# Kernel tuning notes

Measured on AMD Instinct MI355X. Metric: run time of the kernel, lower is better.

The kernel has to match this reference:

```python
import jax, jax.numpy as jnp
import numpy as np

N = 100000
IN_DIM = 128
OUT_DIM = 128
E = 320000


def setup_inputs() -> dict:
    key = jax.random.key(0)
    ks = jax.random.split(key, 12)
    x = jax.random.normal(ks[0], (N, IN_DIM), dtype=jnp.float32)
    src0 = jax.random.randint(ks[1], (E,), 0, N)
    dst0 = jax.random.randint(ks[2], (E,), 0, N)
    src1 = jax.random.randint(ks[3], (E,), 0, N)
    dst1 = jax.random.randint(ks[4], (E,), 0, N)
    s = 1.0 / np.sqrt(IN_DIM)
    W0 = jax.random.uniform(ks[5], (IN_DIM, OUT_DIM), minval=-s, maxval=s)
    b0 = jax.random.uniform(ks[6], (OUT_DIM,), minval=-s, maxval=s)
    W1 = jax.random.uniform(ks[7], (IN_DIM, OUT_DIM), minval=-s, maxval=s)
    b1 = jax.random.uniform(ks[8], (OUT_DIM,), minval=-s, maxval=s)
    sa = 1.0 / np.sqrt(2 * OUT_DIM)
    a0 = jax.random.uniform(ks[9], (2 * OUT_DIM,), minval=-sa, maxval=sa)
    a1 = jax.random.uniform(ks[10], (2 * OUT_DIM,), minval=-sa, maxval=sa)
    return {"x": x, "src0": src0, "dst0": dst0, "src1": src1, "dst1": dst1,
            "W0": W0, "b0": b0, "a0": a0, "W1": W1, "b1": b1, "a1": a1}


def _rel_gat(x, src, dst, W, b, a):
    # wh = Linear(in_dim, out_dim)(x)  -> [N, D]
    wh = x @ W + b
    D = wh.shape[1]
    # e = leaky_relu(a^T [wh_src || wh_dst]) ; split a instead of concat on edges
    e = jax.nn.leaky_relu(wh[src] @ a[:D] + wh[dst] @ a[D:])  # [E]
    # segment softmax over incoming edges of each dst node
    m = jax.ops.segment_max(e, dst, num_segments=N)
    ex = jnp.exp(e - m[dst])
    denom = jax.ops.segment_sum(ex, dst, num_segments=N)
    alpha = ex / denom[dst]  # [E]
    # weighted scatter-sum of src features (zero for isolated dst nodes)
    return jax.ops.segment_sum(alpha[:, None] * wh[src], dst, num_segments=N)


def reference(x, src0, dst0, src1, dst1, W0, b0, a0, W1, b1, a1):
    h0 = _rel_gat(x, src0, dst0, W0, b0, a0)
    h1 = _rel_gat(x, src1, dst1, W1, b1, a1)
    # cross-relation 'sum' reducer
    return h0 + h1
```

## Files before the change

### kernel.cpp

```cpp
#include <hip/hip_runtime.h>
#include <hip/hip_bf16.h>


typedef __bf16 bf16x8 __attribute__((ext_vector_type(8)));
typedef float f32x4 __attribute__((ext_vector_type(4)));

#define DIM 128

__global__ __launch_bounds__(256) void prep_w_kernel(
    const float* __restrict__ W0, const float* __restrict__ W1,
    __bf16* __restrict__ wtf)
{
    const int e = blockIdx.x * 256 + threadIdx.x;
    if (e >= 4096) return;
    const int lane = e & 63;
    const int ko4  = (e >> 6) & 3;
    const int ct   = (e >> 8) & 7;
    const int rel  = e >> 11;
    const float* W = rel ? W1 : W0;
    const int n  = ct * 16 + (lane & 15);
    const int k0 = ko4 * 32 + (lane >> 4) * 8;
    bf16x8 v;
#pragma unroll
    for (int j = 0; j < 8; ++j) v[j] = (__bf16)W[(k0 + j) * DIM + n];
    *(bf16x8*)(wtf + (size_t)e * 8) = v;
}

__global__ __launch_bounds__(256) void gemm_wh_kernel(
    const float* __restrict__ x, const __bf16* __restrict__ wtf,
    const float* __restrict__ b0, const float* __restrict__ b1,
    const float* __restrict__ a0, const float* __restrict__ a1,
    const int* __restrict__ dst0, const int* __restrict__ dst1,
    unsigned* __restrict__ deg, unsigned* __restrict__ rank,
    __bf16* __restrict__ wh, float* __restrict__ s_src,
    float* __restrict__ s_dst, int N, int E)
{
    __shared__ __align__(16) __bf16 Cst[64 * 136];
    const int tid = threadIdx.x;

    {
        const int gid = blockIdx.x * 256 + tid;
        if (gid < E) {
            rank[gid]     = atomicAdd(deg + dst0[gid], 1u);
            rank[E + gid] = atomicAdd(deg + N + dst1[gid], 1u);
        }
    }

    const int lane = tid & 63;
    const int wave = tid >> 6;
    const int quad = lane >> 4;
    const int mr   = lane & 15;

    const long row0 = (long)blockIdx.x * 64 + wave * 16;
    long arow = row0 + mr;
    if (arow >= N) arow = N - 1;
    const f32x4* xr = (const f32x4*)(x + arow * DIM);

    bf16x8 afrag[4];
#pragma unroll
    for (int ko4 = 0; ko4 < 4; ++ko4) {
        f32x4 lo = xr[ko4 * 8 + quad * 2], hi = xr[ko4 * 8 + quad * 2 + 1];
        afrag[ko4] = (bf16x8){ (__bf16)lo.x, (__bf16)lo.y, (__bf16)lo.z, (__bf16)lo.w,
                               (__bf16)hi.x, (__bf16)hi.y, (__bf16)hi.z, (__bf16)hi.w };
    }

    const bf16x8* wt = (const bf16x8*)wtf;

#pragma unroll
    for (int rel = 0; rel < 2; ++rel) {
        f32x4 zero = {0.f, 0.f, 0.f, 0.f};
        f32x4 acc[8];
#pragma unroll
        for (int t = 0; t < 8; ++t) acc[t] = zero;

#pragma unroll
        for (int ko4 = 0; ko4 < 4; ++ko4) {
#pragma unroll
            for (int ct = 0; ct < 8; ++ct) {
                bf16x8 bfrag = wt[((rel * 8 + ct) * 4 + ko4) * 64 + lane];
                acc[ct] = __builtin_amdgcn_mfma_f32_16x16x32_bf16(afrag[ko4], bfrag, acc[ct], 0, 0, 0);
            }
        }

        const float* bias = rel ? b1 : b0;
        const float* a    = rel ? a1 : a0;
        float psr[4] = {0.f, 0.f, 0.f, 0.f};
        float pdr[4] = {0.f, 0.f, 0.f, 0.f};
#pragma unroll
        for (int ct = 0; ct < 8; ++ct) {
            const int c = ct * 16 + mr;
            const float bn = bias[c];
            const float asc = a[c], adc = a[DIM + c];
#pragma unroll
            for (int rr = 0; rr < 4; ++rr) {
                const float wv = acc[ct][rr] + bn;
                Cst[(wave * 16 + quad * 4 + rr) * 136 + c] = (__bf16)wv;
                psr[rr] += asc * wv;
                pdr[rr] += adc * wv;
            }
        }
#pragma unroll
        for (int off = 1; off < 16; off <<= 1) {
#pragma unroll
            for (int rr = 0; rr < 4; ++rr) {
                psr[rr] += __shfl_xor(psr[rr], off);
                pdr[rr] += __shfl_xor(pdr[rr], off);
            }
        }
        if (mr == 0) {
#pragma unroll
            for (int rr = 0; rr < 4; ++rr) {
                const long orow = row0 + quad * 4 + rr;
                if (orow < N) {
                    s_src[(size_t)rel * N + orow] = psr[rr];
                    s_dst[(size_t)rel * N + orow] = pdr[rr];
                }
            }
        }
        __syncthreads();
#pragma unroll
        for (int i = 0; i < 4; ++i) {
            const int chunk = tid + 256 * i;
            const int row = chunk >> 4, c8 = chunk & 15;
            bf16x8 v = *(const bf16x8*)&Cst[row * 136 + c8 * 8];
            const long grow = (long)blockIdx.x * 64 + row;
            if (grow < N)
                *(bf16x8*)(wh + ((size_t)rel * N + grow) * DIM + c8 * 8) = v;
        }
        __syncthreads();
    }
}

__global__ __launch_bounds__(256) void scanA_kernel(
    const unsigned* __restrict__ deg, unsigned* __restrict__ tmp,
    unsigned* __restrict__ bsum, int n)
{
    __shared__ unsigned s[256];
    const int t = threadIdx.x;
    const int i = blockIdx.x * 256 + t;
    unsigned v = (i < n) ? deg[i] : 0u;
    s[t] = v;
    __syncthreads();
#pragma unroll
    for (int off = 1; off < 256; off <<= 1) {
        unsigned add = (t >= off) ? s[t - off] : 0u;
        __syncthreads();
        s[t] += add;
        __syncthreads();
    }
    if (i < n) tmp[i] = s[t] - v;
    if (t == 255) bsum[blockIdx.x] = s[t];
}

__global__ __launch_bounds__(256) void scan2_kernel(
    const unsigned* __restrict__ tmp, const unsigned* __restrict__ bsum,
    const unsigned* __restrict__ deg, unsigned* __restrict__ rowptr,
    int n, int nb)
{
    __shared__ unsigned s[256];
    __shared__ unsigned ex[1024];
    const int t = threadIdx.x;
    unsigned loc[4], sum = 0u;
#pragma unroll
    for (int k = 0; k < 4; ++k) {
        int idx = t * 4 + k;
        loc[k] = (idx < nb) ? bsum[idx] : 0u;
        sum += loc[k];
    }
    s[t] = sum;
    __syncthreads();
#pragma unroll
    for (int off = 1; off < 256; off <<= 1) {
        unsigned add = (t >= off) ? s[t - off] : 0u;
        __syncthreads();
        s[t] += add;
        __syncthreads();
    }
    unsigned run = s[t] - sum;
#pragma unroll
    for (int k = 0; k < 4; ++k) {
        ex[t * 4 + k] = run;
        run += loc[k];
    }
    __syncthreads();
    const unsigned pref = ex[blockIdx.x];
    const int i = blockIdx.x * 256 + t;
    if (i < n) {
        unsigned val = tmp[i] + pref;
        rowptr[i] = val;
        if (i == n - 1) rowptr[n] = val + deg[i];
    }
}

__global__ __launch_bounds__(256) void fill_kernel(
    const int* __restrict__ src0, const int* __restrict__ dst0,
    const int* __restrict__ src1, const int* __restrict__ dst1,
    const float* __restrict__ s_src, const float* __restrict__ s_dst,
    const unsigned* __restrict__ rowptr, const unsigned* __restrict__ rank,
    float* __restrict__ denom, uint2* __restrict__ sorted, int N, int E)
{
    const int i = blockIdx.x * 256 + threadIdx.x;
    if (i >= E) return;
    const int s0 = src0[i], d0 = dst0[i];
    const int s1 = src1[i], d1 = dst1[i];
    const unsigned r0 = rank[i], r1 = rank[E + i];
    const unsigned p0 = rowptr[d0] + r0;
    const unsigned p1 = rowptr[N + d1] + r1;

    float v0 = s_src[s0] + s_dst[d0];
    v0 = v0 > 0.f ? v0 : 0.01f * v0;
    const float e0 = __expf(v0);
    float v1 = s_src[N + s1] + s_dst[N + d1];
    v1 = v1 > 0.f ? v1 : 0.01f * v1;
    const float e1 = __expf(v1);

    sorted[p0] = make_uint2((unsigned)s0, __float_as_uint(e0));
    sorted[p1] = make_uint2((unsigned)s1, __float_as_uint(e1));
    atomicAdd(denom + d0, e0);
    atomicAdd(denom + N + d1, e1);
}

__global__ __launch_bounds__(256) void aggregate_kernel(
    const unsigned* __restrict__ rowptr, const uint2* __restrict__ sorted,
    const float* __restrict__ denom, const __bf16* __restrict__ wh,
    float* __restrict__ out, int N)
{
    const int tid  = threadIdx.x;
    const int lane = tid & 63;
    const int sub  = lane >> 4;
    const int mr   = lane & 15;
    int d = blockIdx.x * 4 + (tid >> 6);
    if (d >= N) return;
    d = __builtin_amdgcn_readfirstlane(d);

    const unsigned beg0 = rowptr[d],     end0 = rowptr[d + 1];
    const unsigned beg1 = rowptr[N + d], end1 = rowptr[N + d + 1];
    const unsigned len0 = end0 - beg0;
    const unsigned T    = len0 + (end1 - beg1);
    const float inv0 = (end0 > beg0) ? 1.f / denom[d]     : 0.f;
    const float inv1 = (end1 > beg1) ? 1.f / denom[N + d] : 0.f;

    float o[8];
#pragma unroll
    for (int k = 0; k < 8; ++k) o[k] = 0.f;

    const size_t whstride = (size_t)N * DIM;

    for (unsigned t0 = 0; t0 < T; t0 += 8) {
        const unsigned tA = t0 + sub, tB = tA + 4;
        const bool vA = tA < T, vB = tB < T;
        const bool rA = tA >= len0, rB = tB >= len0;

        unsigned iA = rA ? beg1 + (tA - len0) : beg0 + tA;
        unsigned iB = rB ? beg1 + (tB - len0) : beg0 + tB;
        iA = vA ? iA : 0u;
        iB = vB ? iB : 0u;

        const uint2 eA = sorted[iA];
        const uint2 eB = sorted[iB];

        const float wgtA = vA ? __uint_as_float(eA.y) * (rA ? inv1 : inv0) : 0.f;
        const float wgtB = vB ? __uint_as_float(eB.y) * (rB ? inv1 : inv0) : 0.f;

        const bf16x8 wA = *(const bf16x8*)(wh + (rA ? whstride : 0)
                                              + (size_t)eA.x * DIM + mr * 8);
        const bf16x8 wB = *(const bf16x8*)(wh + (rB ? whstride : 0)
                                              + (size_t)eB.x * DIM + mr * 8);
#pragma unroll
        for (int k = 0; k < 8; ++k) o[k] += wgtA * (float)wA[k];
#pragma unroll
        for (int k = 0; k < 8; ++k) o[k] += wgtB * (float)wB[k];
    }

#pragma unroll
    for (int k = 0; k < 8; ++k) {
        o[k] += __shfl_xor(o[k], 16);
        o[k] += __shfl_xor(o[k], 32);
    }

    if (sub == 0) {
        float4 v0 = {o[0], o[1], o[2], o[3]};
        float4 v1 = {o[4], o[5], o[6], o[7]};
        float* op = out + (size_t)d * DIM + mr * 8;
        *(float4*)op       = v0;
        *(float4*)(op + 4) = v1;
    }
}

extern "C" void kernel_launch(void* const* d_in, const int* in_sizes, int n_in,
                              void* d_out, int out_size, void* d_ws, size_t ws_size,
                              hipStream_t stream) {
    const float* x = (const float*)d_in[0];
    const int* srcs[2] = {(const int*)d_in[1], (const int*)d_in[3]};
    const int* dsts[2] = {(const int*)d_in[2], (const int*)d_in[4]};
    const float* Ws[2] = {(const float*)d_in[5], (const float*)d_in[8]};
    const float* Bs[2] = {(const float*)d_in[6], (const float*)d_in[9]};
    const float* As[2] = {(const float*)d_in[7], (const float*)d_in[10]};

    const int N = in_sizes[0] / DIM;
    const int E = in_sizes[1];
    const int n2 = 2 * N;
    const int nb = (n2 + 255) / 256;
    float* out = (float*)d_out;

    char* p = (char*)d_ws;
    __bf16*   wh     = (__bf16*)p;   p += (size_t)n2 * DIM * 2;
    __bf16*   wtf    = (__bf16*)p;   p += (size_t)4096 * 8 * 2;
    float*    s_src  = (float*)p;    p += (size_t)n2 * 4;
    float*    s_dst  = (float*)p;    p += (size_t)n2 * 4;
    unsigned* deg    = (unsigned*)p; p += (size_t)n2 * 4;
    float*    denom  = (float*)p;    p += (size_t)n2 * 4;
    unsigned* tmp    = (unsigned*)p; p += (size_t)n2 * 4;
    unsigned* rowptr = (unsigned*)p; p += (size_t)(n2 + 2) * 4;
    unsigned* rank   = (unsigned*)p; p += (size_t)2 * E * 4;
    uint2*    sorted = (uint2*)p;    p += (size_t)2 * E * 8;
    unsigned* bsum   = (unsigned*)p; p += (size_t)nb * 4;

    hipMemsetAsync(deg, 0, (size_t)n2 * 4 * 2, stream);
    prep_w_kernel<<<16, 256, 0, stream>>>(Ws[0], Ws[1], wtf);

    gemm_wh_kernel<<<(N + 63) / 64, 256, 0, stream>>>(
        x, wtf, Bs[0], Bs[1], As[0], As[1],
        dsts[0], dsts[1], deg, rank, wh, s_src, s_dst, N, E);

    scanA_kernel<<<nb, 256, 0, stream>>>(deg, tmp, bsum, n2);
    scan2_kernel<<<nb, 256, 0, stream>>>(tmp, bsum, deg, rowptr, n2, nb);
    fill_kernel<<<(E + 255) / 256, 256, 0, stream>>>(
        srcs[0], dsts[0], srcs[1], dsts[1], s_src, s_dst,
        rowptr, rank, denom, sorted, N, E);
    aggregate_kernel<<<(N + 3) / 4, 256, 0, stream>>>(
        rowptr, sorted, denom, wh, out, N);
}
```

Baseline: 245.8 us.

## Compute softmax denominators in aggregate and pad degree counters to avoid contention

The float atomicAdd denominator pass in fill_kernel is removed. Each aggregate wave now sums exp weights per relation in registers and normalizes at the end, which needs two accumulator sets. The degree counters are also spread to one per 64-byte slot (SPREAD=16), meant to cut atomic contention and false sharing. In exchange the memset and scan read a 16x larger strided buffer, and aggregate holds more registers.

```diff
diff --git a/kernel.cpp b/kernel.cpp
--- a/kernel.cpp
+++ b/kernel.cpp
@@ -6,6 +6,7 @@
 typedef float f32x4 __attribute__((ext_vector_type(4)));
 
 #define DIM 128
+#define SPREAD 16
 
 __global__ __launch_bounds__(256) void prep_w_kernel(
     const float* __restrict__ W0, const float* __restrict__ W1,
@@ -41,8 +42,8 @@
     {
         const int gid = blockIdx.x * 256 + tid;
         if (gid < E) {
-            rank[gid]     = atomicAdd(deg + dst0[gid], 1u);
-            rank[E + gid] = atomicAdd(deg + N + dst1[gid], 1u);
+            rank[gid]     = atomicAdd(deg + (size_t)dst0[gid] * SPREAD, 1u);
+            rank[E + gid] = atomicAdd(deg + ((size_t)N + dst1[gid]) * SPREAD, 1u);
         }
     }
 
@@ -138,7 +139,7 @@
     __shared__ unsigned s[256];
     const int t = threadIdx.x;
     const int i = blockIdx.x * 256 + t;
-    unsigned v = (i < n) ? deg[i] : 0u;
+    unsigned v = (i < n) ? deg[(size_t)i * SPREAD] : 0u;
     s[t] = v;
     __syncthreads();
 #pragma unroll
@@ -188,7 +189,7 @@
     if (i < n) {
         unsigned val = tmp[i] + pref;
         rowptr[i] = val;
-        if (i == n - 1) rowptr[n] = val + deg[i];
+        if (i == n - 1) rowptr[n] = val + deg[(size_t)i * SPREAD];
     }
 }
 
@@ -197,15 +198,14 @@
     const int* __restrict__ src1, const int* __restrict__ dst1,
     const float* __restrict__ s_src, const float* __restrict__ s_dst,
     const unsigned* __restrict__ rowptr, const unsigned* __restrict__ rank,
-    float* __restrict__ denom, uint2* __restrict__ sorted, int N, int E)
+    uint2* __restrict__ sorted, int N, int E)
 {
     const int i = blockIdx.x * 256 + threadIdx.x;
     if (i >= E) return;
     const int s0 = src0[i], d0 = dst0[i];
     const int s1 = src1[i], d1 = dst1[i];
-    const unsigned r0 = rank[i], r1 = rank[E + i];
-    const unsigned p0 = rowptr[d0] + r0;
-    const unsigned p1 = rowptr[N + d1] + r1;
+    const unsigned p0 = rowptr[d0] + rank[i];
+    const unsigned p1 = rowptr[N + d1] + rank[E + i];
 
     float v0 = s_src[s0] + s_dst[d0];
     v0 = v0 > 0.f ? v0 : 0.01f * v0;
@@ -216,14 +216,11 @@
 
     sorted[p0] = make_uint2((unsigned)s0, __float_as_uint(e0));
     sorted[p1] = make_uint2((unsigned)s1, __float_as_uint(e1));
-    atomicAdd(denom + d0, e0);
-    atomicAdd(denom + N + d1, e1);
 }
 
 __global__ __launch_bounds__(256) void aggregate_kernel(
     const unsigned* __restrict__ rowptr, const uint2* __restrict__ sorted,
-    const float* __restrict__ denom, const __bf16* __restrict__ wh,
-    float* __restrict__ out, int N)
+    const __bf16* __restrict__ wh, float* __restrict__ out, int N)
 {
     const int tid  = threadIdx.x;
     const int lane = tid & 63;
@@ -237,12 +234,10 @@
     const unsigned beg1 = rowptr[N + d], end1 = rowptr[N + d + 1];
     const unsigned len0 = end0 - beg0;
     const unsigned T    = len0 + (end1 - beg1);
-    const float inv0 = (end0 > beg0) ? 1.f / denom[d]     : 0.f;
-    const float inv1 = (end1 > beg1) ? 1.f / denom[N + d] : 0.f;
-
-    float o[8];
-#pragma unroll
-    for (int k = 0; k < 8; ++k) o[k] = 0.f;
+
+    float acc0[8], acc1[8], l0 = 0.f, l1 = 0.f;
+#pragma unroll
+    for (int k = 0; k < 8; ++k) { acc0[k] = 0.f; acc1[k] = 0.f; }
 
     const size_t whstride = (size_t)N * DIM;
 
@@ -259,26 +254,42 @@
         const uint2 eA = sorted[iA];
         const uint2 eB = sorted[iB];
 
-        const float wgtA = vA ? __uint_as_float(eA.y) * (rA ? inv1 : inv0) : 0.f;
-        const float wgtB = vB ? __uint_as_float(eB.y) * (rB ? inv1 : inv0) : 0.f;
+        const float evA = vA ? __uint_as_float(eA.y) : 0.f;
+        const float evB = vB ? __uint_as_float(eB.y) : 0.f;
+        const float wA0 = rA ? 0.f : evA, wA1 = rA ? evA : 0.f;
+        const float wB0 = rB ? 0.f : evB, wB1 = rB ? evB : 0.f;
+        l0 += wA0 + wB0;
+        l1 += wA1 + wB1;
 
         const bf16x8 wA = *(const bf16x8*)(wh + (rA ? whstride : 0)
                                               + (size_t)eA.x * DIM + mr * 8);
         const bf16x8 wB = *(const bf16x8*)(wh + (rB ? whstride : 0)
                                               + (size_t)eB.x * DIM + mr * 8);
 #pragma unroll
-        for (int k = 0; k < 8; ++k) o[k] += wgtA * (float)wA[k];
-#pragma unroll
-        for (int k = 0; k < 8; ++k) o[k] += wgtB * (float)wB[k];
+        for (int k = 0; k < 8; ++k) {
+            const float fA = (float)wA[k], fB = (float)wB[k];
+            acc0[k] += wA0 * fA + wB0 * fB;
+            acc1[k] += wA1 * fA + wB1 * fB;
+        }
     }
 
 #pragma unroll
     for (int k = 0; k < 8; ++k) {
-        o[k] += __shfl_xor(o[k], 16);
-        o[k] += __shfl_xor(o[k], 32);
-    }
+        acc0[k] += __shfl_xor(acc0[k], 16);
+        acc0[k] += __shfl_xor(acc0[k], 32);
+        acc1[k] += __shfl_xor(acc1[k], 16);
+        acc1[k] += __shfl_xor(acc1[k], 32);
+    }
+    l0 += __shfl_xor(l0, 16); l0 += __shfl_xor(l0, 32);
+    l1 += __shfl_xor(l1, 16); l1 += __shfl_xor(l1, 32);
+
+    const float inv0 = l0 > 0.f ? 1.f / l0 : 0.f;
+    const float inv1 = l1 > 0.f ? 1.f / l1 : 0.f;
 
     if (sub == 0) {
+        float o[8];
+#pragma unroll
+        for (int k = 0; k < 8; ++k) o[k] = acc0[k] * inv0 + acc1[k] * inv1;
         float4 v0 = {o[0], o[1], o[2], o[3]};
         float4 v1 = {o[4], o[5], o[6], o[7]};
         float* op = out + (size_t)d * DIM + mr * 8;
@@ -308,15 +319,14 @@
     __bf16*   wtf    = (__bf16*)p;   p += (size_t)4096 * 8 * 2;
     float*    s_src  = (float*)p;    p += (size_t)n2 * 4;
     float*    s_dst  = (float*)p;    p += (size_t)n2 * 4;
-    unsigned* deg    = (unsigned*)p; p += (size_t)n2 * 4;
-    float*    denom  = (float*)p;    p += (size_t)n2 * 4;
+    unsigned* deg    = (unsigned*)p; p += (size_t)n2 * SPREAD * 4;
     unsigned* tmp    = (unsigned*)p; p += (size_t)n2 * 4;
     unsigned* rowptr = (unsigned*)p; p += (size_t)(n2 + 2) * 4;
     unsigned* rank   = (unsigned*)p; p += (size_t)2 * E * 4;
     uint2*    sorted = (uint2*)p;    p += (size_t)2 * E * 8;
     unsigned* bsum   = (unsigned*)p; p += (size_t)nb * 4;
 
-    hipMemsetAsync(deg, 0, (size_t)n2 * 4 * 2, stream);
+    hipMemsetAsync(deg, 0, (size_t)n2 * SPREAD * 4, stream);
     prep_w_kernel<<<16, 256, 0, stream>>>(Ws[0], Ws[1], wtf);
 
     gemm_wh_kernel<<<(N + 63) / 64, 256, 0, stream>>>(
@@ -327,7 +337,7 @@
     scan2_kernel<<<nb, 256, 0, stream>>>(tmp, bsum, deg, rowptr, n2, nb);
     fill_kernel<<<(E + 255) / 256, 256, 0, stream>>>(
         srcs[0], dsts[0], srcs[1], dsts[1], s_src, s_dst,
-        rowptr, rank, denom, sorted, N, E);
+        rowptr, rank, sorted, N, E);
     aggregate_kernel<<<(N + 3) / 4, 256, 0, stream>>>(
-        rowptr, sorted, denom, wh, out, N);
-}
+        rowptr, sorted, wh, out, N);
+}
```

Result: faster. 232.2 us (-5.5%).
